# Optimization experiments

Measured on AMD Instinct MI355X. Metric: run time of the kernel, lower is better.

The kernel has to match this reference:

```python
import jax, jax.numpy as jnp
import numpy as np

_EPS = 1e-5
_I48 = float(1.0 / np.sqrt(48.0))
_I16 = float(1.0 / np.sqrt(16.0))
# fully-connected TP paths (mul_in, mul_out) for hidden(48x0e+48x1o+16x1e) x sh(0e+1e+2e) -> hidden
_PATHS = [(48, 48), (48, 16), (48, 48), (48, 48), (48, 48), (16, 16), (16, 48), (16, 16), (16, 16)]
_NW = sum(i * o for i, o in _PATHS)  # 11520


def _ln(x, g, b):
    mu = x.mean(-1, keepdims=True)
    var = ((x - mu) ** 2).mean(-1, keepdims=True)
    return g * (x - mu) * jax.lax.rsqrt(var + _EPS) + b


def _split(W):
    out, off = [], 0
    for i, o in _PATHS:
        out.append(W[:, off:off + i * o].reshape(-1, i, o))
        off += i * o
    return out


def _forward(protein_coords, protein_features, ligand_coords, ligand_features, t,
             te_w1, te_b1, te_w2, te_b2, te_ln_g, te_ln_b,
             pe_w1, pe_b1, pe_ln_g, pe_ln_b, pe_w2, pe_b2,
             le_w1, le_b1, le_ln_g, le_ln_b, le_w2, le_b2,
             sp_w, sp_b, emb_w, ee_w1, ee_b1, ee_w2, ee_b2,
             conv_w1, conv_b1, conv_w2, conv_b2, conv_w3, conv_b3,
             bn_gs, bn_bs, bn_gv, bn_gw, si_ws, si_wv, si_ww,
             out_ws, out_wv, edge_src, edge_dst):
    Nl = ligand_coords.shape[0]
    Np = protein_coords.shape[0]
    N = Nl + Np
    E = edge_src.shape[0]
    silu = jax.nn.silu

    # sinusoidal time embedding -> Linear/SiLU/Linear/LayerNorm
    half = 32
    freq = jnp.exp(jnp.arange(half, dtype=jnp.float32) * (-np.log(10000.0) / (half - 1)))
    emb = t[:, None] * freq[None, :]
    emb = jnp.concatenate([jnp.sin(emb), jnp.cos(emb)], -1)  # (1, 64)
    temb = _ln(silu(emb @ te_w1 + te_b1) @ te_w2 + te_b2, te_ln_g, te_ln_b)

    # scalar node encoders (dropout = eval identity)
    protein_ca = protein_coords[:, 0, :]
    ph = silu(_ln(protein_features @ pe_w1 + pe_b1, pe_ln_g, pe_ln_b)) @ pe_w2 + pe_b2
    lh = silu(_ln(ligand_features @ le_w1 + le_b1, le_ln_g, le_ln_b)) @ le_w2 + le_b2

    # edge geometry (ligand -> protein) + spherical harmonics in Cartesian form
    vec = ligand_coords[edge_src] - protein_ca[edge_dst]  # (E, 3)
    dist = jnp.sqrt((vec ** 2).sum(-1) + 1e-12)
    n = vec / dist[:, None]  # unit vector = l=1 SH
    Q = n[:, :, None] * n[:, None, :] - jnp.eye(3, dtype=n.dtype) / 3.0  # l=2 SH (traceless sym)
    te_exp = jnp.broadcast_to(temb[0], (E, temb.shape[-1]))
    ef = silu(jnp.concatenate([dist[:, None], te_exp], -1) @ ee_w1 + ee_b1) @ ee_w2 + ee_b2  # (E, 32)

    # input embedding: scalars only feed 0e; 1o/1e channels start at zero
    comb = jnp.concatenate([lh, ph], 0) @ sp_w + sp_b  # (N, 48)
    s = (comb @ emb_w) * _I48
    v = jnp.zeros((N, 48, 3), s.dtype)
    w = jnp.zeros((N, 16, 3), s.dtype)

    dst_n = edge_dst + Nl
    deg = jax.ops.segment_sum(jnp.ones((E,), s.dtype), dst_n, N).clip(1.0)

    for i in range(conv_w1.shape[0]):
        # edge MLP -> per-edge fully-connected tensor-product weights
        m = silu(ef @ conv_w1[i] + conv_b1[i])
        m = silu(m @ conv_w2[i] + conv_b2[i])
        Wt = m @ conv_w3[i] + conv_b3[i]  # (E, 11520)
        Wss, Wsw, Wv0, Wv1, Wv2, Ww0, Wws, Ww1, Ww2 = _split(Wt)

        se, ve, we = s[edge_src], v[edge_src], w[edge_src]
        wn = jnp.einsum('eid,ed->ei', we, n)        # 1e x 1e -> 0e (dot)
        cv = jnp.cross(ve, n[:, None, :])           # 1o x 1e -> 1o (cross)
        cw = jnp.cross(we, n[:, None, :])           # 1e x 1e -> 1e (cross)
        qv = jnp.einsum('edc,eic->eid', Q, ve)      # 1o x 2e -> 1o
        qw = jnp.einsum('edc,eic->eid', Q, we)      # 1e x 2e -> 1e

        m_s = jnp.einsum('eio,ei->eo', Wss, se) * _I48 + jnp.einsum('eio,ei->eo', Wws, wn) * _I16
        m_v = (jnp.einsum('eio,eid->eod', Wv0, ve) + jnp.einsum('eio,eid->eod', Wv1, cv)
               + jnp.einsum('eio,eid->eod', Wv2, qv)) * _I48
        m_w = jnp.einsum('eio,ei,ed->eod', Wsw, se, n) * _I48 + (
            jnp.einsum('eio,eid->eod', Ww0, we) + jnp.einsum('eio,eid->eod', Ww1, cw)
            + jnp.einsum('eio,eid->eod', Ww2, qw)) * _I16

        # scatter-mean to destination nodes
        S = jax.ops.segment_sum(m_s, dst_n, N) / deg[:, None]
        V = jax.ops.segment_sum(m_v, dst_n, N) / deg[:, None, None]
        Wm = jax.ops.segment_sum(m_w, dst_n, N) / deg[:, None, None]

        # self interaction (per-irrep linear)
        a_s = S + (s @ si_ws[i]) * _I48
        a_v = V + jnp.einsum('io,nid->nod', si_wv[i], v) * _I48
        a_w = Wm + jnp.einsum('io,nid->nod', si_ww[i], w) * _I16

        # equivariant batch norm (batch statistics)
        mu = a_s.mean(0)
        var = ((a_s - mu) ** 2).mean(0)
        n_s = bn_gs[i] * (a_s - mu) * jax.lax.rsqrt(var + _EPS) + bn_bs[i]
        n_v = a_v * (bn_gv[i] * jax.lax.rsqrt((a_v ** 2).sum(-1).mean(0) + _EPS))[None, :, None]
        n_w = a_w * (bn_gw[i] * jax.lax.rsqrt((a_w ** 2).sum(-1).mean(0) + _EPS))[None, :, None]

        s, v, w = s + n_s, v + n_v, w + n_w

    feats = (s[:Nl] @ out_ws) * _I48                          # (Nl, 256)
    out_v = jnp.einsum('io,nid->nod', out_wv, v[:Nl]) * _I48  # (Nl, 3, 3)
    vf = out_v.mean(1)                                        # vector_field (Nl, 3)
    return jnp.concatenate([vf, feats], -1)                   # (Nl, 259)


def setup_inputs():
    key = jax.random.key(0)
    ks = iter(jax.random.split(key, 80))
    f32 = jnp.float32

    def nrm(shape, scale=1.0):
        return jax.random.normal(next(ks), shape, f32) * scale

    def lin(fi, fo, lead=()):
        return nrm(lead + (fi, fo), 1.0 / np.sqrt(fi)), jnp.zeros(lead + (fo,), f32)

    Nl, Np, E, L = 2048, 4096, 8192, 6
    inp = {}
    inp['protein_coords'] = nrm((Np, 2, 3), 5.0)
    inp['protein_features'] = nrm((Np, 96))
    inp['ligand_coords'] = nrm((Nl, 3), 5.0)
    inp['ligand_features'] = nrm((Nl, 52))
    inp['t'] = jax.random.uniform(next(ks), (1,), f32)
    inp['te_w1'], inp['te_b1'] = lin(64, 128)
    inp['te_w2'], inp['te_b2'] = lin(128, 64)
    inp['te_ln_g'], inp['te_ln_b'] = jnp.ones((64,), f32), jnp.zeros((64,), f32)
    inp['pe_w1'], inp['pe_b1'] = lin(96, 128)
    inp['pe_ln_g'], inp['pe_ln_b'] = jnp.ones((128,), f32), jnp.zeros((128,), f32)
    inp['pe_w2'], inp['pe_b2'] = lin(128, 48)
    inp['le_w1'], inp['le_b1'] = lin(52, 128)
    inp['le_ln_g'], inp['le_ln_b'] = jnp.ones((128,), f32), jnp.zeros((128,), f32)
    inp['le_w2'], inp['le_b2'] = lin(128, 48)
    inp['sp_w'], inp['sp_b'] = lin(48, 48)
    inp['emb_w'] = nrm((48, 48))
    inp['ee_w1'], inp['ee_b1'] = lin(65, 32)
    inp['ee_w2'], inp['ee_b2'] = lin(32, 32)
    inp['conv_w1'], inp['conv_b1'] = lin(32, 128, (L,))
    inp['conv_w2'], inp['conv_b2'] = lin(128, 128, (L,))
    inp['conv_w3'], inp['conv_b3'] = lin(128, _NW, (L,))
    inp['bn_gs'], inp['bn_bs'] = jnp.ones((L, 48), f32), jnp.zeros((L, 48), f32)
    inp['bn_gv'], inp['bn_gw'] = jnp.ones((L, 48), f32), jnp.ones((L, 16), f32)
    inp['si_ws'] = nrm((L, 48, 48))
    inp['si_wv'] = nrm((L, 48, 48))
    inp['si_ww'] = nrm((L, 16, 16))
    inp['out_ws'] = nrm((48, 256))
    inp['out_wv'] = nrm((48, 3))
    inp['edge_src'] = jax.random.randint(next(ks), (E,), 0, Nl)
    inp['edge_dst'] = jax.random.randint(next(ks), (E,), 0, Np)
    return inp


def reference(protein_coords, protein_features, ligand_coords, ligand_features, t,
              te_w1, te_b1, te_w2, te_b2, te_ln_g, te_ln_b,
              pe_w1, pe_b1, pe_ln_g, pe_ln_b, pe_w2, pe_b2,
              le_w1, le_b1, le_ln_g, le_ln_b, le_w2, le_b2,
              sp_w, sp_b, emb_w, ee_w1, ee_b1, ee_w2, ee_b2,
              conv_w1, conv_b1, conv_w2, conv_b2, conv_w3, conv_b3,
              bn_gs, bn_bs, bn_gv, bn_gw, si_ws, si_wv, si_ww,
              out_ws, out_wv, edge_src, edge_dst):
    return _forward(protein_coords, protein_features, ligand_coords, ligand_features, t,
                    te_w1, te_b1, te_w2, te_b2, te_ln_g, te_ln_b,
                    pe_w1, pe_b1, pe_ln_g, pe_ln_b, pe_w2, pe_b2,
                    le_w1, le_b1, le_ln_g, le_ln_b, le_w2, le_b2,
                    sp_w, sp_b, emb_w, ee_w1, ee_b1, ee_w2, ee_b2,
                    conv_w1, conv_b1, conv_w2, conv_b2, conv_w3, conv_b3,
                    bn_gs, bn_bs, bn_gv, bn_gw, si_ws, si_wv, si_ww,
                    out_ws, out_wv, edge_src, edge_dst)
```

## Files before the change

### kernel.cpp

```cpp
#include <hip/hip_runtime.h>
#include <hip/hip_bf16.h>
#include <math.h>

#define I48 0.14433756729740643f
#define NKB 194
#define KCH 4
#define KSPL 6

typedef __attribute__((ext_vector_type(8))) _Float16 half8;
typedef __attribute__((ext_vector_type(4))) float f32x4;

__device__ __forceinline__ float silu_f(float x){ return x / (1.f + __expf(-x)); }

__global__ void k_temb(const float* __restrict__ t_in,
                       const float* __restrict__ w1, const float* __restrict__ b1,
                       const float* __restrict__ w2, const float* __restrict__ b2,
                       const float* __restrict__ g,  const float* __restrict__ b,
                       float* __restrict__ temb){
  __shared__ float emb[64], h1[128], red[128];
  __shared__ float s_mu, s_rs;
  int t = threadIdx.x;
  float tv = t_in[0];
  if (t < 64){
    int i = t & 31;
    float fr = __expf((float)i * (-9.210340371976184f/31.f));
    float a = tv * fr;
    emb[t] = (t < 32) ? sinf(a) : cosf(a);
  }
  __syncthreads();
  {
    float z = b1[t];
    for (int i=0;i<64;i++) z += emb[i]*w1[i*128+t];
    h1[t] = silu_f(z);
  }
  __syncthreads();
  float tp = 0.f;
  if (t < 64){
    tp = b2[t];
    for (int j=0;j<128;j++) tp += h1[j]*w2[j*64+t];
  }
  red[t] = (t<64)? tp : 0.f;
  __syncthreads();
  for (int st=64;st;st>>=1){ if(t<st) red[t]+=red[t+st]; __syncthreads(); }
  if (t==0) s_mu = red[0]/64.f;
  __syncthreads();
  float d = tp - s_mu;
  red[t] = (t<64)? d*d : 0.f;
  __syncthreads();
  for (int st=64;st;st>>=1){ if(t<st) red[t]+=red[t+st]; __syncthreads(); }
  if (t==0) s_rs = rsqrtf(red[0]/64.f + 1e-5f);
  __syncthreads();
  if (t<64) temb[t] = g[t]*(d*s_rs) + b[t];
}

__global__ void k_encs0(const float* __restrict__ x, int in_dim,
                        const float* __restrict__ w1, const float* __restrict__ b1,
                        const float* __restrict__ g,  const float* __restrict__ bb,
                        const float* __restrict__ w2, const float* __restrict__ b2,
                        const float* __restrict__ spw, const float* __restrict__ spb,
                        const float* __restrict__ embw,
                        float* __restrict__ s, int row_off){
  __shared__ float sx[96], sh[128], red[128], vout[48], c48[48];
  __shared__ float s_mu, s_rs;
  int row = blockIdx.x, t = threadIdx.x;
  for (int i=t;i<in_dim;i+=128) sx[i] = x[(size_t)row*in_dim+i];
  __syncthreads();
  float z = b1[t];
  for (int i=0;i<in_dim;i++) z += sx[i]*w1[i*128+t];
  red[t]=z; __syncthreads();
  for (int st=64;st;st>>=1){ if(t<st) red[t]+=red[t+st]; __syncthreads(); }
  if(!t) s_mu = red[0]/128.f;
  __syncthreads();
  float d = z - s_mu;
  red[t]=d*d; __syncthreads();
  for (int st=64;st;st>>=1){ if(t<st) red[t]+=red[t+st]; __syncthreads(); }
  if(!t) s_rs = rsqrtf(red[0]/128.f+1e-5f);
  __syncthreads();
  float h = g[t]*(d*s_rs)+bb[t];
  sh[t] = silu_f(h);
  __syncthreads();
  if (t<48){
    float o = b2[t];
    for (int j=0;j<128;j++) o += sh[j]*w2[j*48+t];
    vout[t] = o;
  }
  __syncthreads();
  if (t<48){
    float c = spb[t];
    for (int i=0;i<48;i++) c += vout[i]*spw[i*48+t];
    c48[t] = c;
  }
  __syncthreads();
  if (t<48){
    float v = 0.f;
    for (int i=0;i<48;i++) v += c48[i]*embw[i*48+t];
    s[(size_t)(row_off+row)*48+t] = v*I48;
  }
}

__global__ void k_edge(const float* __restrict__ lc, const float* __restrict__ pc,
                       const int* __restrict__ src, const int* __restrict__ dst,
                       const float* __restrict__ temb,
                       const float* __restrict__ w1, const float* __restrict__ b1,
                       const float* __restrict__ w2, const float* __restrict__ b2,
                       float* __restrict__ ef, float* __restrict__ degf,
                       int E, int Nl){
  __shared__ float sh_h[2][32];
  int t = threadIdx.x, sub = t>>5, j = t&31;
  int e = blockIdx.x*2 + sub;
  if (e < E){
    int s_ = src[e], d_ = dst[e];
    float vx = lc[(size_t)s_*3+0]-pc[(size_t)d_*6+0];
    float vy = lc[(size_t)s_*3+1]-pc[(size_t)d_*6+1];
    float vz = lc[(size_t)s_*3+2]-pc[(size_t)d_*6+2];
    float dist = sqrtf(vx*vx+vy*vy+vz*vz+1e-12f);
    float h = b1[j] + dist*w1[j];
    for (int a=0;a<64;a++) h += temb[a]*w1[(a+1)*32+j];
    sh_h[sub][j] = silu_f(h);
  }
  __syncthreads();
  if (e < E){
    float o = b2[j];
    for (int a=0;a<32;a++) o += sh_h[sub][a]*w2[a*32+j];
    ef[(size_t)e*32+j] = o;
    if (j==0) atomicAdd(&degf[Nl + dst[e]], 1.f);
  }
}

__global__ void k_packMLP(const float* __restrict__ w1, const float* __restrict__ w2,
                          _Float16* __restrict__ w1p, _Float16* __restrict__ w2p, int L){
  int tot1 = L*8*512;
  int tot2 = L*32*512;
  int total = tot1 + tot2;
  for (int idx = blockIdx.x*blockDim.x+threadIdx.x; idx < total; idx += gridDim.x*blockDim.x){
    if (idx < tot1){
      int j = idx & 7, lane = (idx>>3)&63, rest = idx>>9;
      int nt = rest & 7, l = rest >> 3;
      int k = (lane>>4)*8 + j, o = nt*16 + (lane&15);
      w1p[idx] = (_Float16)w1[((size_t)l*32 + k)*128 + o];
    } else {
      int i2 = idx - tot1;
      int j = i2 & 7, lane = (i2>>3)&63, rest = i2>>9;
      int nt = rest & 7, kb = (rest>>3)&3, l = rest >> 5;
      int k = kb*32 + (lane>>4)*8 + j, o = nt*16 + (lane&15);
      w2p[i2] = (_Float16)w2[((size_t)l*128 + k)*128 + o];
    }
  }
}

__global__ __launch_bounds__(256) void k_mlp2(
    const float* __restrict__ ef,
    const _Float16* __restrict__ w1p, const float* __restrict__ b1a,
    const _Float16* __restrict__ w2p, const float* __restrict__ b2a,
    _Float16* __restrict__ m2h, int E){
  __shared__ __align__(16) _Float16 sef[64][40];
  __shared__ __align__(16) _Float16 shh[64][136];
  __shared__ float sb1[128], sb2[128];
  const int t = threadIdx.x, lane = t & 63, w = t >> 6;
  const int e0 = blockIdx.x * 64;
  const int l  = blockIdx.y;
  const _Float16* w1l = w1p + (size_t)l*4096;
  const _Float16* w2l = w2p + (size_t)l*16384;
  if (t < 128) sb1[t] = b1a[l*128 + t];
  else         sb2[t-128] = b2a[l*128 + (t-128)];
  {
    int row = t >> 2, g = t & 3;
    const float* p = ef + ((size_t)(e0+row))*32 + g*8;
    float4 p0 = *(const float4*)p, p1 = *(const float4*)(p+4);
    half8 hv;
    hv[0]=(_Float16)p0.x; hv[1]=(_Float16)p0.y; hv[2]=(_Float16)p0.z; hv[3]=(_Float16)p0.w;
    hv[4]=(_Float16)p1.x; hv[5]=(_Float16)p1.y; hv[6]=(_Float16)p1.z; hv[7]=(_Float16)p1.w;
    *(half8*)&sef[row][g*8] = hv;
  }
  __syncthreads();
  const int m = lane & 15, quad = lane >> 4;
  const int r = w*16 + m;
  half8 a1 = *(const half8*)&sef[r][quad*8];
  f32x4 acc1[8];
  #pragma unroll
  for (int nt=0; nt<8; nt++){
    half8 b = *(const half8*)(w1l + (nt*64 + lane)*8);
    f32x4 z = {0.f,0.f,0.f,0.f};
    acc1[nt] = __builtin_amdgcn_mfma_f32_16x16x32_f16(a1, b, z, 0,0,0);
  }
  #pragma unroll
  for (int nt=0; nt<8; nt++){
    float bv = sb1[nt*16 + m];
    #pragma unroll
    for (int rr=0; rr<4; rr++)
      shh[w*16 + quad*4 + rr][nt*16 + m] = (_Float16)silu_f(acc1[nt][rr] + bv);
  }
  __syncthreads();
  f32x4 acc2[8];
  #pragma unroll
  for (int nt=0;nt<8;nt++) acc2[nt] = (f32x4){0.f,0.f,0.f,0.f};
  #pragma unroll
  for (int kb=0; kb<4; kb++){
    half8 a2 = *(const half8*)&shh[r][kb*32 + quad*8];
    #pragma unroll
    for (int nt=0; nt<8; nt++){
      half8 b = *(const half8*)(w2l + ((size_t)(kb*8+nt)*64 + lane)*8);
      acc2[nt] = __builtin_amdgcn_mfma_f32_16x16x32_f16(a2, b, acc2[nt], 0,0,0);
    }
  }
  __syncthreads();
  #pragma unroll
  for (int nt=0; nt<8; nt++){
    float bv = sb2[nt*16 + m];
    #pragma unroll
    for (int rr=0; rr<4; rr++)
      shh[w*16 + quad*4 + rr][nt*16 + m] = (_Float16)silu_f(acc2[nt][rr] + bv);
  }
  __syncthreads();
  for (int q = t; q < 64*16; q += 256){
    int row = q >> 4, c = q & 15;
    half8 hv = *(const half8*)&shh[row][c*8];
    *(half8*)(m2h + ((size_t)l*E + e0 + row)*128 + c*8) = hv;
  }
}

__global__ void k_packB2(const float* __restrict__ w3, const float* __restrict__ b3,
                         _Float16* __restrict__ wbh, int L){
  int tot1 = L*128*2304;
  int tot2 = L*64*48;
  int total = tot1 + tot2;
  for (int idx = blockIdx.x*blockDim.x+threadIdx.x; idx < total; idx += gridDim.x*blockDim.x){
    if (idx < tot1){
      int r = idx % 2304; int q = idx / 2304;
      int kk = q & 127;   int l = q >> 7;
      float v = w3[(size_t)(l*128+kk)*11520 + r];
      int i = r / 48, o = r - i*48;
      int kp = i*128 + kk;
      int kblk = kp >> 5, p = kp & 31;
      int lane = ((p>>3)<<4) + (o & 15);
      int j = p & 7;
      int nt = o >> 4;
      wbh[((((size_t)l*NKB + kblk)*3 + nt)*64 + lane)*8 + j] = (_Float16)v;
    } else {
      int i2 = idx - tot1;
      int o = i2 % 48; int q = i2 / 48;
      int ii = q & 63; int l = q >> 6;
      float v = (ii < 48) ? b3[(size_t)l*11520 + ii*48 + o] : 0.f;
      int kp = 6144 + ii;
      int kblk = kp >> 5, p = kp & 31;
      int lane = ((p>>3)<<4) + (o & 15);
      int j = p & 7;
      int nt = o >> 4;
      wbh[((((size_t)l*NKB + kblk)*3 + nt)*64 + lane)*8 + j] = (_Float16)v;
    }
  }
}

__global__ __launch_bounds__(256) void k_msg5(
    const _Float16* __restrict__ m2h, const float* __restrict__ s,
    const _Float16* __restrict__ wbh,
    const int* __restrict__ src, const int* __restrict__ dst,
    float* __restrict__ Sacc, int Nl){
  __shared__ __align__(16) _Float16 sB[2][KCH*1536];
  __shared__ __align__(16) _Float16 sseq[128][72];
  __shared__ int sdst[128];
  const int t = threadIdx.x, lane = t & 63, w = t >> 6;
  const int e0 = blockIdx.x * 128;
  const int by = blockIdx.y;
  const int kb0 = by*32;
  const int kb1 = (by==KSPL-1) ? NKB : kb0+32;

  for (int q = t; q < 128*9; q += 256){
    int e = q/9, g = q - e*9;
    half8 hv = {};
    if (g < 6){
      const float* sp = s + (size_t)src[e0+e]*48 + g*8;
      float4 p0 = *(const float4*)sp, p1 = *(const float4*)(sp+4);
      hv[0]=(_Float16)p0.x; hv[1]=(_Float16)p0.y; hv[2]=(_Float16)p0.z; hv[3]=(_Float16)p0.w;
      hv[4]=(_Float16)p1.x; hv[5]=(_Float16)p1.y; hv[6]=(_Float16)p1.z; hv[7]=(_Float16)p1.w;
    }
    *(half8*)&sseq[e][g*8] = hv;
  }
  if (t < 128) sdst[t] = dst[e0+t];

  const int m = lane & 15, quad = lane >> 4;
  const int r0 = w*32 + m, r1 = r0 + 16;

  half8 f0[4], f1[4];
  {
    const _Float16* base0 = m2h + (size_t)(e0+r0)*128 + quad*8;
    const _Float16* base1 = m2h + (size_t)(e0+r1)*128 + quad*8;
    #pragma unroll
    for (int sub=0; sub<4; sub++){
      f0[sub] = *(const half8*)(base0 + sub*32);
      f1[sub] = *(const half8*)(base1 + sub*32);
    }
  }

  auto stage = [&](int c){
    int kbase = kb0 + c*KCH;
    int nk = kb1 - kbase; if (nk > KCH) nk = KCH;
    int bytes = nk*3072;
    const char* g = (const char*)wbh + (size_t)kbase*3072;
    char* lb = (char*)sB[c&1];
    for (int off = w*1024; off < bytes; off += 4096){
      __builtin_amdgcn_global_load_lds(
        (const __attribute__((address_space(1))) void*)(g + off + (size_t)lane*16),
        (__attribute__((address_space(3))) void*)(lb + off), 16, 0, 0);
    }
  };
  stage(0);

  f32x4 acc00={0.f,0.f,0.f,0.f}, acc01={0.f,0.f,0.f,0.f}, acc02={0.f,0.f,0.f,0.f};
  f32x4 acc10={0.f,0.f,0.f,0.f}, acc11={0.f,0.f,0.f,0.f}, acc12={0.f,0.f,0.f,0.f};

  const int nch = (kb1-kb0+KCH-1)/KCH;
  for (int c = 0; c < nch; c++){
    __syncthreads();
    if (c+1 < nch) stage(c+1);
    int kbase = kb0 + c*KCH;
    int kbn = kb1 - kbase; if (kbn > KCH) kbn = KCH;
    const _Float16* bb = sB[c&1];
    if (kbn == KCH && kbase < 192){
      int i = kbase >> 2;
      _Float16 sv0 = sseq[r0][i], sv1 = sseq[r1][i];
      half8 s0v = {sv0,sv0,sv0,sv0,sv0,sv0,sv0,sv0};
      half8 s1v = {sv1,sv1,sv1,sv1,sv1,sv1,sv1,sv1};
      #pragma unroll
      for (int kk = 0; kk < KCH; kk++){
        half8 a0 = f0[kk] * s0v;
        half8 a1 = f1[kk] * s1v;
        const _Float16* bk = bb + kk*1536 + lane*8;
        half8 b0 = *(const half8*)(bk);
        half8 b1 = *(const half8*)(bk + 512);
        half8 b2 = *(const half8*)(bk + 1024);
        acc00 = __builtin_amdgcn_mfma_f32_16x16x32_f16(a0, b0, acc00, 0, 0, 0);
        acc01 = __builtin_amdgcn_mfma_f32_16x16x32_f16(a0, b1, acc01, 0, 0, 0);
        acc02 = __builtin_amdgcn_mfma_f32_16x16x32_f16(a0, b2, acc02, 0, 0, 0);
        acc10 = __builtin_amdgcn_mfma_f32_16x16x32_f16(a1, b0, acc10, 0, 0, 0);
        acc11 = __builtin_amdgcn_mfma_f32_16x16x32_f16(a1, b1, acc11, 0, 0, 0);
        acc12 = __builtin_amdgcn_mfma_f32_16x16x32_f16(a1, b2, acc12, 0, 0, 0);
      }
    } else {
      for (int kk = 0; kk < kbn; kk++){
        int kblk = kbase + kk;
        int ib = ((kblk-192) << 5) + quad*8;
        half8 a0 = *(const half8*)&sseq[r0][ib];
        half8 a1 = *(const half8*)&sseq[r1][ib];
        const _Float16* bk = bb + kk*1536 + lane*8;
        half8 b0 = *(const half8*)(bk);
        half8 b1 = *(const half8*)(bk + 512);
        half8 b2 = *(const half8*)(bk + 1024);
        acc00 = __builtin_amdgcn_mfma_f32_16x16x32_f16(a0, b0, acc00, 0, 0, 0);
        acc01 = __builtin_amdgcn_mfma_f32_16x16x32_f16(a0, b1, acc01, 0, 0, 0);
        acc02 = __builtin_amdgcn_mfma_f32_16x16x32_f16(a0, b2, acc02, 0, 0, 0);
        acc10 = __builtin_amdgcn_mfma_f32_16x16x32_f16(a1, b0, acc10, 0, 0, 0);
        acc11 = __builtin_amdgcn_mfma_f32_16x16x32_f16(a1, b1, acc11, 0, 0, 0);
        acc12 = __builtin_amdgcn_mfma_f32_16x16x32_f16(a1, b2, acc12, 0, 0, 0);
      }
    }
  }
  #pragma unroll
  for (int r = 0; r < 4; r++){
    int el0 = w*32 + quad*4 + r;
    int el1 = el0 + 16;
    float* p0 = Sacc + (size_t)(Nl + sdst[el0])*48 + m;
    float* p1 = Sacc + (size_t)(Nl + sdst[el1])*48 + m;
    atomicAdd(p0 +  0, acc00[r]*I48);
    atomicAdd(p0 + 16, acc01[r]*I48);
    atomicAdd(p0 + 32, acc02[r]*I48);
    atomicAdd(p1 +  0, acc10[r]*I48);
    atomicAdd(p1 + 16, acc11[r]*I48);
    atomicAdd(p1 + 32, acc12[r]*I48);
  }
}

__global__ __launch_bounds__(256) void k_node2(const float* __restrict__ Sacc,
                       const float* __restrict__ degf,
                       const float* __restrict__ s, const float* __restrict__ siw,
                       float* __restrict__ a_s, float* __restrict__ bnl, int N){
  __shared__ float sh_s[16][48];
  __shared__ float sw[2304];
  __shared__ float csum[48], csq[48];
  int t = threadIdx.x;
  int n0 = blockIdx.x*16;
  for (int q=t;q<2304;q+=256) sw[q] = siw[q];
  for (int q=t;q<768;q+=256){
    int nl=q/48, i=q-nl*48;
    sh_s[nl][i] = s[(size_t)(n0+nl)*48+i];
  }
  if (t<48){ csum[t]=0.f; csq[t]=0.f; }
  __syncthreads();
  int nl = t>>4;
  int ob = (t&15)*3;
  int n = n0+nl;
  float dg = degf[n]; if (dg < 1.f) dg = 1.f;
  float inv = 1.f/dg;
  #pragma unroll
  for (int j=0;j<3;j++){
    int o = ob+j;
    float acc = 0.f;
    for (int i=0;i<48;i++) acc += sh_s[nl][i]*sw[i*48+o];
    float a = Sacc[(size_t)n*48+o]*inv + acc*I48;
    a_s[(size_t)n*48+o] = a;
    atomicAdd(&csum[o], a);
    atomicAdd(&csq[o], a*a);
  }
  __syncthreads();
  if (t<96) atomicAdd(&bnl[t], (t<48) ? csum[t] : csq[t-48]);
}

__global__ __launch_bounds__(256) void k_supd3(
    float* __restrict__ s, float* __restrict__ Sacc,
    const float* __restrict__ a_s, const float* __restrict__ bnl,
    const float* __restrict__ g, const float* __restrict__ b, int N){
  __shared__ float ksc[48], kbs[48];
  int t = threadIdx.x;
  if (t < 48){
    float su = bnl[t], sq = bnl[48+t];
    float mu  = su/(float)N;
    float var = sq/(float)N - mu*mu;
    float r = rsqrtf(var + 1e-5f);
    float sc = g[t]*r;
    ksc[t] = sc;
    kbs[t] = b[t] - mu*sc;
  }
  __syncthreads();
  size_t base = (size_t)blockIdx.x*768;
  for (int q=t; q<768; q+=256){
    int o = q % 48;
    size_t idx = base + q;
    s[idx] += a_s[idx]*ksc[o] + kbs[o];
    Sacc[idx] = 0.f;
  }
}

__global__ void k_out(const float* __restrict__ s, const float* __restrict__ ows,
                      float* __restrict__ out){
  __shared__ float sh_s[48];
  int n = blockIdx.x, t = threadIdx.x;
  if (t<48) sh_s[t] = s[(size_t)n*48+t];
  __syncthreads();
  float acc = 0.f;
  for (int i=0;i<48;i++) acc += sh_s[i]*ows[i*256+t];
  out[(size_t)n*259 + 3 + t] = acc*I48;
  if (t<3) out[(size_t)n*259 + t] = 0.f;
}

extern "C" void kernel_launch(void* const* d_in, const int* in_sizes, int n_in,
                              void* d_out, int out_size, void* d_ws, size_t ws_size,
                              hipStream_t stream){
  const float* protein_coords   = (const float*)d_in[0];
  const float* protein_features = (const float*)d_in[1];
  const float* ligand_coords    = (const float*)d_in[2];
  const float* ligand_features  = (const float*)d_in[3];
  const float* t_in    = (const float*)d_in[4];
  const float* te_w1   = (const float*)d_in[5];
  const float* te_b1   = (const float*)d_in[6];
  const float* te_w2   = (const float*)d_in[7];
  const float* te_b2   = (const float*)d_in[8];
  const float* te_ln_g = (const float*)d_in[9];
  const float* te_ln_b = (const float*)d_in[10];
  const float* pe_w1   = (const float*)d_in[11];
  const float* pe_b1   = (const float*)d_in[12];
  const float* pe_ln_g = (const float*)d_in[13];
  const float* pe_ln_b = (const float*)d_in[14];
  const float* pe_w2   = (const float*)d_in[15];
  const float* pe_b2   = (const float*)d_in[16];
  const float* le_w1   = (const float*)d_in[17];
  const float* le_b1   = (const float*)d_in[18];
  const float* le_ln_g = (const float*)d_in[19];
  const float* le_ln_b = (const float*)d_in[20];
  const float* le_w2   = (const float*)d_in[21];
  const float* le_b2   = (const float*)d_in[22];
  const float* sp_w    = (const float*)d_in[23];
  const float* sp_b    = (const float*)d_in[24];
  const float* emb_w   = (const float*)d_in[25];
  const float* ee_w1   = (const float*)d_in[26];
  const float* ee_b1   = (const float*)d_in[27];
  const float* ee_w2   = (const float*)d_in[28];
  const float* ee_b2   = (const float*)d_in[29];
  const float* conv_w1 = (const float*)d_in[30];
  const float* conv_b1 = (const float*)d_in[31];
  const float* conv_w2 = (const float*)d_in[32];
  const float* conv_b2 = (const float*)d_in[33];
  const float* conv_w3 = (const float*)d_in[34];
  const float* conv_b3 = (const float*)d_in[35];
  const float* bn_gs   = (const float*)d_in[36];
  const float* bn_bs   = (const float*)d_in[37];
  const float* si_ws   = (const float*)d_in[40];
  const float* out_ws  = (const float*)d_in[43];
  const int* edge_src  = (const int*)d_in[45];
  const int* edge_dst  = (const int*)d_in[46];

  int Np = in_sizes[0]/6;
  int Nl = in_sizes[2]/3;
  int E  = in_sizes[45];
  int N  = Nl+Np;
  int L  = in_sizes[36]/48;

  float* W = (float*)d_ws;
  size_t off = 0;
  auto alloc = [&](size_t n)->float*{ float* p = W+off; off += (n+63)&~(size_t)63; return p; };
  float* degf  = alloc(N);
  float* Sacc  = alloc((size_t)N*48);
  float* bnb   = alloc((size_t)L*96);
  float* temb  = alloc(64);
  float* sbuf  = alloc((size_t)N*48);
  float* ef    = alloc((size_t)E*32);
  float* a_s   = alloc((size_t)N*48);
  _Float16* m2h = (_Float16*)alloc((size_t)L*E*128/2 + 64);
  _Float16* wbh = (_Float16*)alloc((size_t)L*NKB*1536/2 + 64);
  _Float16* w1p = (_Float16*)alloc((size_t)L*4096/2 + 64);
  _Float16* w2p = (_Float16*)alloc((size_t)L*16384/2 + 64);

  hipMemsetAsync(degf, 0, ((size_t)N + (size_t)N*48 + (size_t)L*96 + 192)*sizeof(float), stream);
  k_packB2<<<2048,256,0,stream>>>(conv_w3, conv_b3, wbh, L);
  k_packMLP<<<480,256,0,stream>>>(conv_w1, conv_w2, w1p, w2p, L);
  k_temb<<<1,128,0,stream>>>(t_in, te_w1, te_b1, te_w2, te_b2, te_ln_g, te_ln_b, temb);
  k_encs0<<<Np,128,0,stream>>>(protein_features, 96, pe_w1, pe_b1, pe_ln_g, pe_ln_b,
                               pe_w2, pe_b2, sp_w, sp_b, emb_w, sbuf, Nl);
  k_encs0<<<Nl,128,0,stream>>>(ligand_features, 52, le_w1, le_b1, le_ln_g, le_ln_b,
                               le_w2, le_b2, sp_w, sp_b, emb_w, sbuf, 0);
  k_edge<<<(E+1)/2,64,0,stream>>>(ligand_coords, protein_coords, edge_src, edge_dst, temb,
                                  ee_w1, ee_b1, ee_w2, ee_b2, ef, degf, E, Nl);
  dim3 mlpg(E/64, L);
  k_mlp2<<<mlpg,256,0,stream>>>(ef, w1p, conv_b1, w2p, conv_b2, m2h, E);

  dim3 mgrid(E/128, KSPL);
  for (int l=0;l<L;l++){
    k_msg5<<<mgrid,256,0,stream>>>(m2h + (size_t)l*E*128, sbuf, wbh + (size_t)l*NKB*1536,
                                   edge_src, edge_dst, Sacc, Nl);
    k_node2<<<N/16,256,0,stream>>>(Sacc, degf, sbuf, si_ws + (size_t)l*2304, a_s, bnb + l*96, N);
    k_supd3<<<N/16,256,0,stream>>>(sbuf, Sacc, a_s, bnb + l*96, bn_gs + l*48, bn_bs + l*48, N);
  }
  k_out<<<Nl,256,0,stream>>>(sbuf, out_ws, (float*)d_out);
}
```

Baseline: 471.1 us.

## Fuse batchnorm state update into next layer's message and node kernels

Removes the separate k_supd3 launch per layer. The previous layer's batchnorm affine update is now applied on the fly: inside k_msg6 when gathering source features, and inside k_node3, which also writes the updated s and zeroes Sacc. The final layer's update moves into k_out2. This cuts one launch and one full pass over s/a_s per layer, at the cost of recomputing BN scale/shift in every block and doing extra scalar loads of a_s in the gather.

After: 463.1 us. About the same (-1.7%).

```diff
diff --git a/kernel.cpp b/kernel.cpp
--- a/kernel.cpp
+++ b/kernel.cpp
@@ -251,32 +251,56 @@
   }
 }
 
-__global__ __launch_bounds__(256) void k_msg5(
+__global__ __launch_bounds__(256) void k_msg6(
     const _Float16* __restrict__ m2h, const float* __restrict__ s,
+    const float* __restrict__ a_s, const float* __restrict__ bnlp,
+    const float* __restrict__ gp, const float* __restrict__ bp, int apply, int N,
     const _Float16* __restrict__ wbh,
     const int* __restrict__ src, const int* __restrict__ dst,
     float* __restrict__ Sacc, int Nl){
   __shared__ __align__(16) _Float16 sB[2][KCH*1536];
   __shared__ __align__(16) _Float16 sseq[128][72];
   __shared__ int sdst[128];
+  __shared__ float ksc[48], kbs[48];
   const int t = threadIdx.x, lane = t & 63, w = t >> 6;
   const int e0 = blockIdx.x * 128;
   const int by = blockIdx.y;
   const int kb0 = by*32;
   const int kb1 = (by==KSPL-1) ? NKB : kb0+32;
 
+  if (t < 48){
+    if (apply){
+      float su = bnlp[t], sq = bnlp[48+t];
+      float mu  = su/(float)N;
+      float var = sq/(float)N - mu*mu;
+      float r = rsqrtf(var + 1e-5f);
+      float sc = gp[t]*r;
+      ksc[t] = sc; kbs[t] = bp[t] - mu*sc;
+    } else { ksc[t]=0.f; kbs[t]=0.f; }
+  }
+  if (t < 128) sdst[t] = dst[e0+t];
+  __syncthreads();
+
   for (int q = t; q < 128*9; q += 256){
     int e = q/9, g = q - e*9;
     half8 hv = {};
     if (g < 6){
-      const float* sp = s + (size_t)src[e0+e]*48 + g*8;
-      float4 p0 = *(const float4*)sp, p1 = *(const float4*)(sp+4);
-      hv[0]=(_Float16)p0.x; hv[1]=(_Float16)p0.y; hv[2]=(_Float16)p0.z; hv[3]=(_Float16)p0.w;
-      hv[4]=(_Float16)p1.x; hv[5]=(_Float16)p1.y; hv[6]=(_Float16)p1.z; hv[7]=(_Float16)p1.w;
+      size_t base = (size_t)src[e0+e]*48 + g*8;
+      const float* sp = s + base;
+      if (apply){
+        const float* ap = a_s + base;
+        #pragma unroll
+        for (int j=0;j<8;j++){
+          int o = g*8+j;
+          hv[j] = (_Float16)(sp[j] + ap[j]*ksc[o] + kbs[o]);
+        }
+      } else {
+        #pragma unroll
+        for (int j=0;j<8;j++) hv[j] = (_Float16)sp[j];
+      }
     }
     *(half8*)&sseq[e][g*8] = hv;
   }
-  if (t < 128) sdst[t] = dst[e0+t];
 
   const int m = lane & 15, quad = lane >> 4;
   const int r0 = w*32 + m, r1 = r0 + 16;
@@ -370,21 +394,42 @@
   }
 }
 
-__global__ __launch_bounds__(256) void k_node2(const float* __restrict__ Sacc,
+__global__ __launch_bounds__(256) void k_node3(float* __restrict__ Sacc,
                        const float* __restrict__ degf,
-                       const float* __restrict__ s, const float* __restrict__ siw,
-                       float* __restrict__ a_s, float* __restrict__ bnl, int N){
+                       float* __restrict__ s, const float* __restrict__ siw,
+                       float* __restrict__ a_s,
+                       const float* __restrict__ bnlp, const float* __restrict__ gp,
+                       const float* __restrict__ bp, int apply,
+                       float* __restrict__ bnl, int N){
   __shared__ float sh_s[16][48];
   __shared__ float sw[2304];
   __shared__ float csum[48], csq[48];
+  __shared__ float ksc[48], kbs[48];
   int t = threadIdx.x;
   int n0 = blockIdx.x*16;
+  if (t < 48){
+    if (apply){
+      float su = bnlp[t], sq = bnlp[48+t];
+      float mu  = su/(float)N;
+      float var = sq/(float)N - mu*mu;
+      float r = rsqrtf(var + 1e-5f);
+      float sc = gp[t]*r;
+      ksc[t] = sc; kbs[t] = bp[t] - mu*sc;
+    } else { ksc[t]=0.f; kbs[t]=0.f; }
+    csum[t]=0.f; csq[t]=0.f;
+  }
   for (int q=t;q<2304;q+=256) sw[q] = siw[q];
+  __syncthreads();
   for (int q=t;q<768;q+=256){
-    int nl=q/48, i=q-nl*48;
-    sh_s[nl][i] = s[(size_t)(n0+nl)*48+i];
-  }
-  if (t<48){ csum[t]=0.f; csq[t]=0.f; }
+    int nl=q/48, o=q-nl*48;
+    size_t idx = (size_t)(n0+nl)*48+o;
+    float v = s[idx];
+    if (apply){
+      v += a_s[idx]*ksc[o] + kbs[o];
+      s[idx] = v;
+    }
+    sh_s[nl][o] = v;
+  }
   __syncthreads();
   int nl = t>>4;
   int ob = (t&15)*3;
@@ -394,10 +439,12 @@
   #pragma unroll
   for (int j=0;j<3;j++){
     int o = ob+j;
+    size_t idx = (size_t)n*48+o;
     float acc = 0.f;
     for (int i=0;i<48;i++) acc += sh_s[nl][i]*sw[i*48+o];
-    float a = Sacc[(size_t)n*48+o]*inv + acc*I48;
-    a_s[(size_t)n*48+o] = a;
+    float a = Sacc[idx]*inv + acc*I48;
+    Sacc[idx] = 0.f;
+    a_s[idx] = a;
     atomicAdd(&csum[o], a);
     atomicAdd(&csq[o], a*a);
   }
@@ -405,36 +452,26 @@
   if (t<96) atomicAdd(&bnl[t], (t<48) ? csum[t] : csq[t-48]);
 }
 
-__global__ __launch_bounds__(256) void k_supd3(
-    float* __restrict__ s, float* __restrict__ Sacc,
-    const float* __restrict__ a_s, const float* __restrict__ bnl,
-    const float* __restrict__ g, const float* __restrict__ b, int N){
+__global__ void k_out2(const float* __restrict__ s, const float* __restrict__ a_s,
+                       const float* __restrict__ bnlp, const float* __restrict__ gp,
+                       const float* __restrict__ bp, int N,
+                       const float* __restrict__ ows, float* __restrict__ out){
+  __shared__ float sh_s[48];
   __shared__ float ksc[48], kbs[48];
-  int t = threadIdx.x;
+  int n = blockIdx.x, t = threadIdx.x;
   if (t < 48){
-    float su = bnl[t], sq = bnl[48+t];
+    float su = bnlp[t], sq = bnlp[48+t];
     float mu  = su/(float)N;
     float var = sq/(float)N - mu*mu;
     float r = rsqrtf(var + 1e-5f);
-    float sc = g[t]*r;
-    ksc[t] = sc;
-    kbs[t] = b[t] - mu*sc;
-  }
-  __syncthreads();
-  size_t base = (size_t)blockIdx.x*768;
-  for (int q=t; q<768; q+=256){
-    int o = q % 48;
-    size_t idx = base + q;
-    s[idx] += a_s[idx]*ksc[o] + kbs[o];
-    Sacc[idx] = 0.f;
-  }
-}
-
-__global__ void k_out(const float* __restrict__ s, const float* __restrict__ ows,
-                      float* __restrict__ out){
-  __shared__ float sh_s[48];
-  int n = blockIdx.x, t = threadIdx.x;
-  if (t<48) sh_s[t] = s[(size_t)n*48+t];
+    float sc = gp[t]*r;
+    ksc[t] = sc; kbs[t] = bp[t] - mu*sc;
+  }
+  __syncthreads();
+  if (t<48){
+    size_t idx = (size_t)n*48+t;
+    sh_s[t] = s[idx] + a_s[idx]*ksc[t] + kbs[t];
+  }
   __syncthreads();
   float acc = 0.f;
   for (int i=0;i<48;i++) acc += sh_s[i]*ows[i*256+t];
@@ -524,10 +561,15 @@
 
   dim3 mgrid(E/128, KSPL);
   for (int l=0;l<L;l++){
-    k_msg5<<<mgrid,256,0,stream>>>(m2h + (size_t)l*E*128, sbuf, wbh + (size_t)l*NKB*1536,
-                                   edge_src, edge_dst, Sacc, Nl);
-    k_node2<<<N/16,256,0,stream>>>(Sacc, degf, sbuf, si_ws + (size_t)l*2304, a_s, bnb + l*96, N);
-    k_supd3<<<N/16,256,0,stream>>>(sbuf, Sacc, a_s, bnb + l*96, bn_gs + l*48, bn_bs + l*48, N);
-  }
-  k_out<<<Nl,256,0,stream>>>(sbuf, out_ws, (float*)d_out);
-}
+    const float* bnlp = (l>0) ? (bnb + (l-1)*96) : bnb;
+    const float* gp   = (l>0) ? (bn_gs + (l-1)*48) : bn_gs;
+    const float* bp   = (l>0) ? (bn_bs + (l-1)*48) : bn_bs;
+    int apply = (l>0) ? 1 : 0;
+    k_msg6<<<mgrid,256,0,stream>>>(m2h + (size_t)l*E*128, sbuf, a_s, bnlp, gp, bp, apply, N,
+                                   wbh + (size_t)l*NKB*1536, edge_src, edge_dst, Sacc, Nl);
+    k_node3<<<N/16,256,0,stream>>>(Sacc, degf, sbuf, si_ws + (size_t)l*2304, a_s,
+                                   bnlp, gp, bp, apply, bnb + l*96, N);
+  }
+  k_out2<<<Nl,256,0,stream>>>(sbuf, a_s, bnb + (L-1)*96, bn_gs + (L-1)*48, bn_bs + (L-1)*48,
+                              N, out_ws, (float*)d_out);
+}
```
